# Optimization experiments

Measured on AMD Instinct MI355X. Metric: run time of the kernel, lower is better.

## Reference

```python
import jax, jax.numpy as jnp
import numpy as np

B, N, D = 16, 1024, 5
R_HID = 8  # radial MLP hidden width


def setup_inputs() -> dict:
    key = jax.random.key(0)
    ks = jax.random.split(key, 16)
    feats = jax.random.normal(ks[0], (B, N, D), jnp.float32)
    coors = 3.0 * jax.random.normal(ks[1], (B, N, 3), jnp.float32)
    a = jax.random.bernoulli(ks[2], 0.01, (B, N, N))
    adj_mat = a | jnp.swapaxes(a, 1, 2)
    s = 1.0 / np.sqrt(D)
    Wq = s * jax.random.normal(ks[3], (D, D), jnp.float32)
    Wk = s * jax.random.normal(ks[4], (D, D), jnp.float32)
    Wv = s * jax.random.normal(ks[5], (D, D), jnp.float32)
    Wo = s * jax.random.normal(ks[6], (D, D), jnp.float32)
    w_r1 = 0.5 * jax.random.normal(ks[7], (1, R_HID), jnp.float32)
    b_r1 = jnp.zeros((R_HID,), jnp.float32)
    w_r2 = 0.5 * jax.random.normal(ks[8], (R_HID, 1), jnp.float32)
    b_r2 = jnp.zeros((1,), jnp.float32)
    w1 = (1.0 / np.sqrt(D)) * jax.random.normal(ks[9], (D, 128), jnp.float32)
    b1 = jnp.zeros((128,), jnp.float32)
    w2 = (1.0 / np.sqrt(128.0)) * jax.random.normal(ks[10], (128, 3), jnp.float32)
    b2 = jnp.zeros((3,), jnp.float32)
    return dict(feats=feats, coors=coors, adj_mat=adj_mat, Wq=Wq, Wk=Wk, Wv=Wv,
                Wo=Wo, w_r1=w_r1, b_r1=b_r1, w_r2=w_r2, b_r2=b_r2,
                w1=w1, b1=b1, w2=w2, b2=b2)


def _se3_layer(feats, coors, neigh, Wq, Wk, Wv, Wo, w_r1, b_r1, w_r2, b_r2):
    # SE(3)-invariant sparse graph attention on degree-0 channels.
    # Attention logits = content term + radial (distance-only) bias, so the
    # scalar output is invariant to global rotations/translations of coors.
    q = jnp.einsum('bnd,de->bne', feats, Wq)
    k = jnp.einsum('bnd,de->bne', feats, Wk)
    v = jnp.einsum('bnd,de->bne', feats, Wv)
    rel = coors[:, :, None, :] - coors[:, None, :, :]        # [B,N,N,3]
    dist = jnp.sqrt(jnp.sum(rel * rel, axis=-1) + 1e-8)      # [B,N,N]
    h = jax.nn.relu(dist[..., None] * w_r1[0] + b_r1)        # [B,N,N,R_HID]
    rbias = (h @ w_r2)[..., 0] + b_r2[0]                     # [B,N,N]
    scores = jnp.einsum('bid,bjd->bij', q, k) / np.sqrt(q.shape[-1]) + rbias
    scores = jnp.where(neigh, scores, -1e9)
    attn = jax.nn.softmax(scores, axis=-1)
    agg = jnp.einsum('bij,bjd->bid', attn, v)
    return feats + jnp.einsum('bid,de->bie', agg, Wo)        # residual


def reference(feats, coors, adj_mat, Wq, Wk, Wv, Wo, w_r1, b_r1, w_r2, b_r2,
              w1, b1, w2, b2):
    a = adj_mat.astype(jnp.float32)
    # num_adj_degrees=2: attend over 1-hop and 2-hop neighbors (+ self)
    adj2 = jnp.einsum('bij,bjk->bik', a, a) > 0
    eye = jnp.eye(adj_mat.shape[1], dtype=bool)[None]
    neigh = adj_mat | adj2 | eye
    x = _se3_layer(feats, coors, neigh, Wq, Wk, Wv, Wo, w_r1, b_r1, w_r2, b_r2)
    pooled = jnp.mean(x, axis=1)                              # [B, D]
    hdn = jax.nn.relu(pooled @ w1 + b1)
    return hdn @ w2 + b2                                      # [B, 3]
```

## Files before the change

### kernel.cpp

```cpp
#include <hip/hip_runtime.h>
#include <hip/hip_bf16.h>

#define BB 16
#define NN 1024
#define DD 5
#define RH 8

typedef unsigned long long u64;
typedef unsigned int u32;
typedef __hip_bfloat16 bf16;

static __device__ __forceinline__ float tof(bf16 x) { return __bfloat162float(x); }
static __device__ __forceinline__ float ldf(const void* p, long long i, bool f) {
  return f ? ((const float*)p)[i] : tof(((const bf16*)p)[i]);
}

#define LOG2E 1.4426950408889634f
#define PACK_BLOCKS (BB * NN * 16 / 256)
#define KV_BLOCKS (BB * NN / 256)

__global__ __launch_bounds__(256) void k_pack(
    const void* __restrict__ adj, const void* __restrict__ feats,
    const void* __restrict__ coors,
    const void* __restrict__ Wk, const void* __restrict__ Wv,
    const void* __restrict__ Wo,
    u64* __restrict__ adjbits, float4* __restrict__ kvg,
    float* __restrict__ czg, int* __restrict__ gflags) {
  __shared__ int sNon01, sNonpair, sLow3;
  __shared__ int sCnt[4];
  __shared__ float wkL[25], wvL[25], woL[25];
  int tid = threadIdx.x;

  if (blockIdx.x >= PACK_BLOCKS) {
    int kb = blockIdx.x - PACK_BLOCKS;
    {
      u32 x = ((const u32*)feats)[tid];
      u32 lo = x & 0xFFFFu;
      int e = (int)((lo >> 7) & 0xFFu);
      bool insane = !(lo == 0u || (e >= 90 && e <= 150));
      u64 m = __ballot(insane);
      if ((tid & 63) == 0) sCnt[tid >> 6] = (int)__popcll(m);
    }
    if (tid < 25) {
    }
    __syncthreads();
    bool f32 = (sCnt[0] + sCnt[1] + sCnt[2] + sCnt[3]) > 64;
    if (tid < 25) {
      wkL[tid] = ldf(Wk, tid, f32);
      wvL[tid] = ldf(Wv, tid, f32);
      woL[tid] = ldf(Wo, tid, f32);
    }
    if (kb == 0 && tid == 0) gflags[0] = f32 ? 1 : 0;
    __syncthreads();
    long long node = (long long)kb * 256 + tid;
    float f0 = ldf(feats, node * DD + 0, f32), f1 = ldf(feats, node * DD + 1, f32),
          f2 = ldf(feats, node * DD + 2, f32), f3 = ldf(feats, node * DD + 3, f32),
          f4 = ldf(feats, node * DD + 4, f32);
    float k[DD], tv[DD], v[DD];
    #pragma unroll
    for (int e = 0; e < DD; ++e) {
      k[e] = f0 * wkL[e] + f1 * wkL[5 + e] + f2 * wkL[10 + e] + f3 * wkL[15 + e] +
             f4 * wkL[20 + e];
      tv[e] = f0 * wvL[e] + f1 * wvL[5 + e] + f2 * wvL[10 + e] + f3 * wvL[15 + e] +
              f4 * wvL[20 + e];
    }
    #pragma unroll
    for (int e = 0; e < DD; ++e)
      v[e] = tv[0] * woL[e] + tv[1] * woL[5 + e] + tv[2] * woL[10 + e] +
             tv[3] * woL[15 + e] + tv[4] * woL[20 + e];
    float cx = ldf(coors, node * 3 + 0, f32);
    float cy = ldf(coors, node * 3 + 1, f32);
    float cz = ldf(coors, node * 3 + 2, f32);
    kvg[node * 3 + 0] = make_float4(k[0], k[1], k[2], k[3]);
    kvg[node * 3 + 1] = make_float4(k[4], v[0], v[1], v[2]);
    kvg[node * 3 + 2] = make_float4(v[3], v[4], cx, cy);
    czg[node] = cz;
    return;
  }

  if (tid == 0) { sNon01 = 0; sNonpair = 0; sLow3 = 0; }
  __syncthreads();
  {
    const u32* aw = (const u32*)adj;
    int non01 = 0, nonpair = 0, low3 = 0;
    for (int i = tid; i < 4096; i += 256) {
      u32 x = aw[i];
      u32 lo = x & 0xFFFFu, hi = x >> 16;
      non01 |= (x > 1u);
      nonpair |= !((lo == 0u || lo == 0x3F80u) && (hi == 0u || hi == 0x3F80u));
      low3 |= (lo == 0x3F80u);
    }
    if (non01) atomicOr(&sNon01, 1);
    if (nonpair) atomicOr(&sNonpair, 1);
    if (low3) atomicOr(&sLow3, 1);
  }
  __syncthreads();
  int mode;
  if (!sNon01) mode = 0;
  else if (!sNonpair) mode = sLow3 ? 2 : 3;
  else mode = 1;

  int gid = blockIdx.x * 256 + tid;
  int w = gid & 15;
  long long row = gid >> 4;
  long long base = row * NN + (long long)w * 64;
  u64 bits = 0;
  if (mode == 3) {
    const uint4* p = (const uint4*)((const float*)adj + base);
    #pragma unroll
    for (int t = 0; t < 16; ++t) {
      uint4 x = p[t];
      if (x.x << 1) bits |= 1ull << (4 * t + 0);
      if (x.y << 1) bits |= 1ull << (4 * t + 1);
      if (x.z << 1) bits |= 1ull << (4 * t + 2);
      if (x.w << 1) bits |= 1ull << (4 * t + 3);
    }
  } else if (mode == 0) {
    const uint4* p = (const uint4*)((const u32*)adj + base);
    #pragma unroll
    for (int t = 0; t < 16; ++t) {
      uint4 x = p[t];
      if (x.x) bits |= 1ull << (4 * t + 0);
      if (x.y) bits |= 1ull << (4 * t + 1);
      if (x.z) bits |= 1ull << (4 * t + 2);
      if (x.w) bits |= 1ull << (4 * t + 3);
    }
  } else if (mode == 2) {
    const uint4* p = (const uint4*)((const unsigned short*)adj + base);
    #pragma unroll
    for (int t = 0; t < 8; ++t) {
      uint4 x = p[t];
      u32 c[4] = {x.x, x.y, x.z, x.w};
      #pragma unroll
      for (int q = 0; q < 4; ++q) {
        if ((c[q] & 0x7FFFu)) bits |= 1ull << (8 * t + 2 * q + 0);
        if ((c[q] >> 16) & 0x7FFFu) bits |= 1ull << (8 * t + 2 * q + 1);
      }
    }
  } else {
    const uint4* p = (const uint4*)((const unsigned char*)adj + base);
    #pragma unroll
    for (int t = 0; t < 4; ++t) {
      uint4 x = p[t];
      u32 c[4] = {x.x, x.y, x.z, x.w};
      #pragma unroll
      for (int q = 0; q < 4; ++q)
        #pragma unroll
        for (int bb = 0; bb < 4; ++bb)
          if ((c[q] >> (8 * bb)) & 0xFFu) bits |= 1ull << (16 * t + 4 * q + bb);
    }
  }
  adjbits[gid] = bits;
}

__global__ __launch_bounds__(256) void k_twohop(const u64* __restrict__ adjbits,
                                                u64* __restrict__ neighbits) {
  __shared__ unsigned short listL[4][NN];
  int wave = threadIdx.x >> 6, lane = threadIdx.x & 63;
  int row = blockIdx.x * 4 + wave;
  int b = row >> 10;
  int i = row & (NN - 1);
  int w = lane & 15;
  const u64* rowp = adjbits + (size_t)row * 16;
  u64 rw = rowp[w];
  unsigned short* list = listL[wave];
  int cnt = 0;
  #pragma unroll
  for (int sw = 0; sw < 16; ++sw) {
    u64 bits = __shfl(rw, sw, 64);
    int mybit = (int)((bits >> lane) & 1ull);
    int pre = __popcll(bits & ((1ull << lane) - 1ull));
    if (mybit) list[cnt + pre] = (unsigned short)(sw * 64 + lane);
    cnt += __popcll(bits);
  }
  __syncthreads();
  u64 acc = rw;
  if (w == (i >> 6)) acc |= 1ull << (i & 63);
  int g = lane >> 4;
  const u64* basep = adjbits + (size_t)b * NN * 16;
  for (int n = g; n < cnt; n += 4) {
    int j = list[n];
    acc |= basep[(size_t)j * 16 + w];
  }
  acc |= __shfl_xor(acc, 16, 64);
  acc |= __shfl_xor(acc, 32, 64);
  if (lane < 16) neighbits[(size_t)row * 16 + lane] = acc;
}

__global__ __launch_bounds__(256) void k_attn(
    const void* __restrict__ feats, const void* __restrict__ coors,
    const void* __restrict__ Wq,
    const void* __restrict__ wr1, const void* __restrict__ br1,
    const void* __restrict__ wr2, const void* __restrict__ br2,
    const float4* __restrict__ kvg, const float* __restrict__ czg,
    const int* __restrict__ gflags,
    const u64* __restrict__ neighbits, float* __restrict__ rowAgg) {
  __shared__ __align__(16) float4 kvL[512 * 3];
  __shared__ float czL[512];
  __shared__ float wqL[25];
  __shared__ float qL[16 * DD], ciL[16 * 3];
  __shared__ float wrL[3][RH];
  __shared__ float sConst[2];
  __shared__ int sFast;
  int bi = blockIdx.x;
  int b = bi >> 7, rem = bi & 127, chunk = rem >> 1, half = rem & 1;
  int j0 = half * 512;
  int tid = threadIdx.x;
  bool f32 = gflags[0] != 0;
  if (tid < 25) wqL[tid] = ldf(Wq, tid, f32);
  if (tid >= 64 && tid < 64 + RH) {
    int h = tid - 64;
    wrL[0][h] = ldf(wr1, h, f32);
    wrL[1][h] = ldf(br1, h, f32);
    wrL[2][h] = ldf(wr2, h, f32);
  }
  if (tid == 96) {
    float c = 0.0f;
    int ok = 1;
    #pragma unroll
    for (int h = 0; h < RH; ++h) {
      float w1h = ldf(wr1, h, f32);
      if (ldf(br1, h, f32) != 0.0f) ok = 0;
      if (w1h > 0.0f) c += w1h * ldf(wr2, h, f32);
    }
    sConst[0] = c * LOG2E;
    sConst[1] = ldf(br2, 0, f32) * LOG2E;
    sFast = ok;
  }
  {
    const float4* src = kvg + ((size_t)(b * NN) + j0) * 3;
    for (int idx = tid; idx < 512 * 3; idx += 256) kvL[idx] = src[idx];
    const float* csrc = czg + (size_t)(b * NN) + j0;
    for (int idx = tid; idx < 512; idx += 256) czL[idx] = csrc[idx];
  }
  __syncthreads();
  int fast = sFast;
  if (tid < 16) {
    long long row = (long long)b * NN + chunk * 16 + tid;
    float f0 = ldf(feats, row * DD + 0, f32), f1 = ldf(feats, row * DD + 1, f32),
          f2 = ldf(feats, row * DD + 2, f32), f3 = ldf(feats, row * DD + 3, f32),
          f4 = ldf(feats, row * DD + 4, f32);
    float qsc = fast ? (0.4472135954999579f * LOG2E) : 0.4472135954999579f;
    #pragma unroll
    for (int e = 0; e < DD; ++e)
      qL[tid * DD + e] = (f0 * wqL[e] + f1 * wqL[5 + e] + f2 * wqL[10 + e] +
                          f3 * wqL[15 + e] + f4 * wqL[20 + e]) * qsc;
    #pragma unroll
    for (int c = 0; c < 3; ++c)
      ciL[tid * 3 + c] = ldf(coors, row * 3 + c, f32);
  }
  __syncthreads();

  int g = tid >> 6, lane = tid & 63;
  int i0 = chunk * 16 + g * 4;
  float q[4][DD], ci[4][3], l[4], A[4][DD];
  #pragma unroll
  for (int r = 0; r < 4; ++r) {
    #pragma unroll
    for (int e = 0; e < DD; ++e) q[r][e] = qL[(g * 4 + r) * DD + e];
    #pragma unroll
    for (int c = 0; c < 3; ++c) ci[r][c] = ciL[(g * 4 + r) * 3 + c];
    l[r] = 0.0f;
    #pragma unroll
    for (int e = 0; e < DD; ++e) A[r][e] = 0.0f;
  }
  const u64* nb = neighbits + ((size_t)(b * NN + i0)) * 16 + half * 8;
  float Cf = sConst[0], br2f = sConst[1];
  for (int it = 0; it < 8; ++it) {
    int j = it * 64 + lane;
    float4 ka = kvL[j * 3 + 0];
    float4 kb = kvL[j * 3 + 1];
    float4 kc = kvL[j * 3 + 2];
    float jx = kc.z, jy = kc.w, jz = czL[j];
    u64 nw[4];
    #pragma unroll
    for (int r = 0; r < 4; ++r) nw[r] = nb[(size_t)r * 16 + it];
    if (fast) {
      #pragma unroll
      for (int r = 0; r < 4; ++r) {
        float cx = jx - ci[r][0], cy = jy - ci[r][1], cz = jz - ci[r][2];
        float dist =
            __builtin_amdgcn_sqrtf(fmaf(cx, cx, fmaf(cy, cy, fmaf(cz, cz, 1e-8f))));
        float s = fmaf(q[r][0], ka.x, br2f);
        s = fmaf(q[r][1], ka.y, s);
        s = fmaf(q[r][2], ka.z, s);
        s = fmaf(q[r][3], ka.w, s);
        s = fmaf(q[r][4], kb.x, s);
        s = fmaf(Cf, dist, s);
        s = fminf(s, 126.0f);
        s = ((nw[r] >> lane) & 1ull) ? s : -150.0f;
        float p = __builtin_amdgcn_exp2f(s);
        l[r] += p;
        A[r][0] = fmaf(p, kb.y, A[r][0]);
        A[r][1] = fmaf(p, kb.z, A[r][1]);
        A[r][2] = fmaf(p, kb.w, A[r][2]);
        A[r][3] = fmaf(p, kc.x, A[r][3]);
        A[r][4] = fmaf(p, kc.y, A[r][4]);
      }
    } else {
      #pragma unroll
      for (int r = 0; r < 4; ++r) {
        float cx = jx - ci[r][0], cy = jy - ci[r][1], cz = jz - ci[r][2];
        float dist = sqrtf(fmaf(cx, cx, fmaf(cy, cy, fmaf(cz, cz, 1e-8f))));
        float rb = ldf(br2, 0, f32);
        #pragma unroll
        for (int h = 0; h < RH; ++h)
          rb += fmaxf(dist * wrL[0][h] + wrL[1][h], 0.0f) * wrL[2][h];
        float s = fmaf(q[r][0], ka.x, rb);
        s = fmaf(q[r][1], ka.y, s);
        s = fmaf(q[r][2], ka.z, s);
        s = fmaf(q[r][3], ka.w, s);
        s = fmaf(q[r][4], kb.x, s);
        s = fminf(s, 85.0f);
        s = ((nw[r] >> lane) & 1ull) ? s : -100.0f;
        float p = __expf(s);
        l[r] += p;
        A[r][0] = fmaf(p, kb.y, A[r][0]);
        A[r][1] = fmaf(p, kb.z, A[r][1]);
        A[r][2] = fmaf(p, kb.w, A[r][2]);
        A[r][3] = fmaf(p, kc.x, A[r][3]);
        A[r][4] = fmaf(p, kc.y, A[r][4]);
      }
    }
  }
  #pragma unroll
  for (int msk = 1; msk < 64; msk <<= 1) {
    #pragma unroll
    for (int r = 0; r < 4; ++r) {
      l[r] += __shfl_xor(l[r], msk, 64);
      A[r][0] += __shfl_xor(A[r][0], msk, 64);
      A[r][1] += __shfl_xor(A[r][1], msk, 64);
      A[r][2] += __shfl_xor(A[r][2], msk, 64);
      A[r][3] += __shfl_xor(A[r][3], msk, 64);
      A[r][4] += __shfl_xor(A[r][4], msk, 64);
    }
  }
  if (lane == 0) {
    #pragma unroll
    for (int r = 0; r < 4; ++r) {
      float* o = rowAgg + (((size_t)(b * NN + i0 + r)) * 2 + half) * 6;
      o[0] = l[r];
      o[1] = A[r][0]; o[2] = A[r][1]; o[3] = A[r][2]; o[4] = A[r][3]; o[5] = A[r][4];
    }
  }
}

__global__ __launch_bounds__(256) void k_final(
    const void* __restrict__ feats, const float* __restrict__ rowAgg,
    const int* __restrict__ gflags,
    const void* __restrict__ w1, const void* __restrict__ b1,
    const void* __restrict__ w2, const void* __restrict__ b2,
    float* __restrict__ out) {
  __shared__ float waveL[4][DD];
  __shared__ float poolL[DD];
  __shared__ float hL[128];
  int b = blockIdx.x, tid = threadIdx.x;
  bool f32 = gflags[0] != 0;
  float pe[DD] = {0.f, 0.f, 0.f, 0.f, 0.f};
  for (int n = tid; n < NN; n += 256) {
    const float* ag = rowAgg + ((size_t)(b * NN + n)) * 12;
    float l = ag[0] + ag[6];
    float inv = (l > 0.f) ? 1.0f / l : 0.0f;
    long long base = ((long long)b * NN + n) * DD;
    #pragma unroll
    for (int e = 0; e < DD; ++e)
      pe[e] += ldf(feats, base + e, f32) + (ag[1 + e] + ag[7 + e]) * inv;
  }
  #pragma unroll
  for (int off = 32; off >= 1; off >>= 1)
    #pragma unroll
    for (int e = 0; e < DD; ++e) pe[e] += __shfl_down(pe[e], off, 64);
  int wave = tid >> 6, lane = tid & 63;
  if (lane == 0)
    #pragma unroll
    for (int e = 0; e < DD; ++e) waveL[wave][e] = pe[e];
  __syncthreads();
  if (tid < DD)
    poolL[tid] = (waveL[0][tid] + waveL[1][tid] + waveL[2][tid] + waveL[3][tid]) *
                 (1.0f / 1024.0f);
  __syncthreads();
  if (tid < 128) {
    float acc = ldf(b1, tid, f32);
    #pragma unroll
    for (int d = 0; d < DD; ++d)
      acc = fmaf(poolL[d], ldf(w1, d * 128 + tid, f32), acc);
    hL[tid] = fmaxf(acc, 0.0f);
  }
  __syncthreads();
  if (tid < 3) {
    float s = ldf(b2, tid, f32);
    for (int j = 0; j < 128; ++j) s = fmaf(hL[j], ldf(w2, j * 3 + tid, f32), s);
    out[b * 3 + tid] = s;
  }
}

extern "C" void kernel_launch(void* const* d_in, const int* in_sizes, int n_in,
                              void* d_out, int out_size, void* d_ws, size_t ws_size,
                              hipStream_t stream) {
  const void* adj = d_in[2];
  float* out = (float*)d_out;

  char* w = (char*)d_ws;
  int* gflags = (int*)w;
  const size_t MB2 = (size_t)BB * NN * 16 * sizeof(u64);
  u64* adjbits = (u64*)(w + 512);
  u64* neighbits = (u64*)(w + 512 + MB2);
  float* rowAgg = (float*)(w + 512 + 2 * MB2);
  float4* kvg = (float4*)(w + 512 + 2 * MB2 + 786432);
  float* czg = (float*)(w + 512 + 2 * MB2 + 2 * 786432);

  k_pack<<<PACK_BLOCKS + KV_BLOCKS, 256, 0, stream>>>(
      adj, d_in[0], d_in[1], d_in[4], d_in[5], d_in[6], adjbits, kvg, czg, gflags);
  k_twohop<<<BB * NN / 4, 256, 0, stream>>>(adjbits, neighbits);
  k_attn<<<BB * 128, 256, 0, stream>>>(d_in[0], d_in[1], d_in[3], d_in[7], d_in[8],
                                       d_in[9], d_in[10], kvg, czg, gflags,
                                       neighbits, rowAgg);
  k_final<<<BB, 256, 0, stream>>>(d_in[0], rowAgg, gflags, d_in[11], d_in[12],
                                  d_in[13], d_in[14], out);
}
```

Measured before the change: 188.1 us.

## Fuse two-hop neighbor mask computation into attention kernel

Removes the separate k_twohop kernel and its neighbits global buffer. Each attention block now computes the two-hop neighbor mask for its own 16 rows and 512-column half directly from adjbits, using the kvL shared buffer as scratch for the neighbor lists before kv data is loaded. This saves one kernel launch and the global write and read of neighbits. In exchange, each row's two-hop OR is recomputed twice, once per column half, and the mask work is serialized ahead of the kv load inside the attention block.

After: 200.2 us. +6.5%, slower.

```diff
diff --git a/kernel.cpp b/kernel.cpp
--- a/kernel.cpp
+++ b/kernel.cpp
@@ -41,8 +41,6 @@
       u64 m = __ballot(insane);
       if ((tid & 63) == 0) sCnt[tid >> 6] = (int)__popcll(m);
     }
-    if (tid < 25) {
-    }
     __syncthreads();
     bool f32 = (sCnt[0] + sCnt[1] + sCnt[2] + sCnt[3]) > 64;
     if (tid < 25) {
@@ -153,50 +151,17 @@
   adjbits[gid] = bits;
 }
 
-__global__ __launch_bounds__(256) void k_twohop(const u64* __restrict__ adjbits,
-                                                u64* __restrict__ neighbits) {
-  __shared__ unsigned short listL[4][NN];
-  int wave = threadIdx.x >> 6, lane = threadIdx.x & 63;
-  int row = blockIdx.x * 4 + wave;
-  int b = row >> 10;
-  int i = row & (NN - 1);
-  int w = lane & 15;
-  const u64* rowp = adjbits + (size_t)row * 16;
-  u64 rw = rowp[w];
-  unsigned short* list = listL[wave];
-  int cnt = 0;
-  #pragma unroll
-  for (int sw = 0; sw < 16; ++sw) {
-    u64 bits = __shfl(rw, sw, 64);
-    int mybit = (int)((bits >> lane) & 1ull);
-    int pre = __popcll(bits & ((1ull << lane) - 1ull));
-    if (mybit) list[cnt + pre] = (unsigned short)(sw * 64 + lane);
-    cnt += __popcll(bits);
-  }
-  __syncthreads();
-  u64 acc = rw;
-  if (w == (i >> 6)) acc |= 1ull << (i & 63);
-  int g = lane >> 4;
-  const u64* basep = adjbits + (size_t)b * NN * 16;
-  for (int n = g; n < cnt; n += 4) {
-    int j = list[n];
-    acc |= basep[(size_t)j * 16 + w];
-  }
-  acc |= __shfl_xor(acc, 16, 64);
-  acc |= __shfl_xor(acc, 32, 64);
-  if (lane < 16) neighbits[(size_t)row * 16 + lane] = acc;
-}
-
 __global__ __launch_bounds__(256) void k_attn(
     const void* __restrict__ feats, const void* __restrict__ coors,
     const void* __restrict__ Wq,
     const void* __restrict__ wr1, const void* __restrict__ br1,
     const void* __restrict__ wr2, const void* __restrict__ br2,
     const float4* __restrict__ kvg, const float* __restrict__ czg,
-    const int* __restrict__ gflags,
-    const u64* __restrict__ neighbits, float* __restrict__ rowAgg) {
+    const int* __restrict__ gflags, const u64* __restrict__ adjbits,
+    float* __restrict__ rowAgg) {
   __shared__ __align__(16) float4 kvL[512 * 3];
   __shared__ float czL[512];
+  __shared__ u64 nbL[16][8];
   __shared__ float wqL[25];
   __shared__ float qL[16 * DD], ciL[16 * 3];
   __shared__ float wrL[3][RH];
@@ -206,6 +171,7 @@
   int b = bi >> 7, rem = bi & 127, chunk = rem >> 1, half = rem & 1;
   int j0 = half * 512;
   int tid = threadIdx.x;
+  int wave = tid >> 6, lane = tid & 63;
   bool f32 = gflags[0] != 0;
   if (tid < 25) wqL[tid] = ldf(Wq, tid, f32);
   if (tid >= 64 && tid < 64 + RH) {
@@ -227,13 +193,44 @@
     sConst[1] = ldf(br2, 0, f32) * LOG2E;
     sFast = ok;
   }
+
+  {
+    unsigned short* list = (unsigned short*)kvL + wave * NN;
+    const u64* basep = adjbits + (size_t)b * NN * 16;
+    int w8 = lane & 7;
+    int widx = half * 8 + w8;
+    for (int rr = 0; rr < 4; ++rr) {
+      int lr = wave * 4 + rr;
+      int i = chunk * 16 + lr;
+      const u64* rowp = basep + (size_t)i * 16;
+      u64 rw = rowp[lane & 15];
+      int cnt = 0;
+      #pragma unroll
+      for (int sw = 0; sw < 16; ++sw) {
+        u64 bits = __shfl(rw, sw, 64);
+        int mybit = (int)((bits >> lane) & 1ull);
+        int pre = __popcll(bits & ((1ull << lane) - 1ull));
+        if (mybit) list[cnt + pre] = (unsigned short)(sw * 64 + lane);
+        cnt += __popcll(bits);
+      }
+      u64 acc = __shfl(rw, widx, 64);
+      if ((i >> 6) == widx) acc |= 1ull << (i & 63);
+      int g8 = lane >> 3;
+      for (int n = g8; n < cnt; n += 8) acc |= basep[(size_t)list[n] * 16 + widx];
+      acc |= __shfl_xor(acc, 8, 64);
+      acc |= __shfl_xor(acc, 16, 64);
+      acc |= __shfl_xor(acc, 32, 64);
+      if (lane < 8) nbL[lr][lane] = acc;
+    }
+  }
+  __syncthreads();
+
   {
     const float4* src = kvg + ((size_t)(b * NN) + j0) * 3;
     for (int idx = tid; idx < 512 * 3; idx += 256) kvL[idx] = src[idx];
     const float* csrc = czg + (size_t)(b * NN) + j0;
     for (int idx = tid; idx < 512; idx += 256) czL[idx] = csrc[idx];
   }
-  __syncthreads();
   int fast = sFast;
   if (tid < 16) {
     long long row = (long long)b * NN + chunk * 16 + tid;
@@ -251,20 +248,18 @@
   }
   __syncthreads();
 
-  int g = tid >> 6, lane = tid & 63;
-  int i0 = chunk * 16 + g * 4;
+  int i0 = chunk * 16 + wave * 4;
   float q[4][DD], ci[4][3], l[4], A[4][DD];
   #pragma unroll
   for (int r = 0; r < 4; ++r) {
     #pragma unroll
-    for (int e = 0; e < DD; ++e) q[r][e] = qL[(g * 4 + r) * DD + e];
-    #pragma unroll
-    for (int c = 0; c < 3; ++c) ci[r][c] = ciL[(g * 4 + r) * 3 + c];
+    for (int e = 0; e < DD; ++e) q[r][e] = qL[(wave * 4 + r) * DD + e];
+    #pragma unroll
+    for (int c = 0; c < 3; ++c) ci[r][c] = ciL[(wave * 4 + r) * 3 + c];
     l[r] = 0.0f;
     #pragma unroll
     for (int e = 0; e < DD; ++e) A[r][e] = 0.0f;
   }
-  const u64* nb = neighbits + ((size_t)(b * NN + i0)) * 16 + half * 8;
   float Cf = sConst[0], br2f = sConst[1];
   for (int it = 0; it < 8; ++it) {
     int j = it * 64 + lane;
@@ -274,7 +269,7 @@
     float jx = kc.z, jy = kc.w, jz = czL[j];
     u64 nw[4];
     #pragma unroll
-    for (int r = 0; r < 4; ++r) nw[r] = nb[(size_t)r * 16 + it];
+    for (int r = 0; r < 4; ++r) nw[r] = nbL[wave * 4 + r][it];
     if (fast) {
       #pragma unroll
       for (int r = 0; r < 4; ++r) {
@@ -404,17 +399,15 @@
   int* gflags = (int*)w;
   const size_t MB2 = (size_t)BB * NN * 16 * sizeof(u64);
   u64* adjbits = (u64*)(w + 512);
-  u64* neighbits = (u64*)(w + 512 + MB2);
-  float* rowAgg = (float*)(w + 512 + 2 * MB2);
-  float4* kvg = (float4*)(w + 512 + 2 * MB2 + 786432);
-  float* czg = (float*)(w + 512 + 2 * MB2 + 2 * 786432);
+  float* rowAgg = (float*)(w + 512 + MB2);
+  float4* kvg = (float4*)(w + 512 + MB2 + 786432);
+  float* czg = (float*)(w + 512 + MB2 + 2 * 786432);
 
   k_pack<<<PACK_BLOCKS + KV_BLOCKS, 256, 0, stream>>>(
       adj, d_in[0], d_in[1], d_in[4], d_in[5], d_in[6], adjbits, kvg, czg, gflags);
-  k_twohop<<<BB * NN / 4, 256, 0, stream>>>(adjbits, neighbits);
   k_attn<<<BB * 128, 256, 0, stream>>>(d_in[0], d_in[1], d_in[3], d_in[7], d_in[8],
                                        d_in[9], d_in[10], kvg, czg, gflags,
-                                       neighbits, rowAgg);
+                                       adjbits, rowAgg);
   k_final<<<BB, 256, 0, stream>>>(d_in[0], rowAgg, gflags, d_in[11], d_in[12],
                                   d_in[13], d_in[14], out);
 }
```

## Fuse final pooling and MLP into attention kernel via last-block counters

Applied to the files above, without the earlier changes.

Removes the separate k_final launch by having the second block of each row-chunk pair combine both halves, reduce its 16 rows and atomically add them into a per-batch pooled buffer. The last block to finish, found through a global done counter, runs the small MLP head for all batches. Counters and the pooled buffer are zeroed in k_pack. This saves one kernel launch and a serial tail kernel, at the cost of extra atomics, fences and a grid-wide last-block pattern. Float atomic accumulation also makes the pooled sum order nondeterministic.

Result: slower. 203.9 us (+8.4%).

```diff
diff --git a/kernel.cpp b/kernel.cpp
--- a/kernel.cpp
+++ b/kernel.cpp
@@ -13,6 +13,12 @@
 static __device__ __forceinline__ float tof(bf16 x) { return __bfloat162float(x); }
 static __device__ __forceinline__ float ldf(const void* p, long long i, bool f) {
   return f ? ((const float*)p)[i] : tof(((const bf16*)p)[i]);
+}
+static __device__ __forceinline__ void stG(float* p, float v) {
+  __hip_atomic_store(p, v, __ATOMIC_RELAXED, __HIP_MEMORY_SCOPE_AGENT);
+}
+static __device__ __forceinline__ float ldG(const float* p) {
+  return __hip_atomic_load(p, __ATOMIC_RELAXED, __HIP_MEMORY_SCOPE_AGENT);
 }
 
 #define LOG2E 1.4426950408889634f
@@ -25,7 +31,9 @@
     const void* __restrict__ Wk, const void* __restrict__ Wv,
     const void* __restrict__ Wo,
     u64* __restrict__ adjbits, float4* __restrict__ kvg,
-    float* __restrict__ czg, int* __restrict__ gflags) {
+    float* __restrict__ czg, int* __restrict__ gflags,
+    int* __restrict__ pairCnt, int* __restrict__ doneCnt,
+    float* __restrict__ pooled) {
   __shared__ int sNon01, sNonpair, sLow3;
   __shared__ int sCnt[4];
   __shared__ float wkL[25], wvL[25], woL[25];
@@ -40,8 +48,6 @@
       bool insane = !(lo == 0u || (e >= 90 && e <= 150));
       u64 m = __ballot(insane);
       if ((tid & 63) == 0) sCnt[tid >> 6] = (int)__popcll(m);
-    }
-    if (tid < 25) {
     }
     __syncthreads();
     bool f32 = (sCnt[0] + sCnt[1] + sCnt[2] + sCnt[3]) > 64;
@@ -78,6 +84,11 @@
     return;
   }
 
+  if (blockIdx.x == 0) {
+    for (int i = tid; i < BB * 64; i += 256) pairCnt[i] = 0;
+    if (tid < BB * DD) pooled[tid] = 0.0f;
+    if (tid == 0) *doneCnt = 0;
+  }
   if (tid == 0) { sNon01 = 0; sNonpair = 0; sLow3 = 0; }
   __syncthreads();
   {
@@ -194,18 +205,24 @@
     const void* __restrict__ wr2, const void* __restrict__ br2,
     const float4* __restrict__ kvg, const float* __restrict__ czg,
     const int* __restrict__ gflags,
-    const u64* __restrict__ neighbits, float* __restrict__ rowAgg) {
+    const u64* __restrict__ neighbits, float* __restrict__ rowAgg,
+    int* __restrict__ pairCnt, int* __restrict__ doneCnt,
+    float* __restrict__ pooled,
+    const void* __restrict__ w1v, const void* __restrict__ b1v,
+    const void* __restrict__ w2v, const void* __restrict__ b2v,
+    float* __restrict__ out) {
   __shared__ __align__(16) float4 kvL[512 * 3];
   __shared__ float czL[512];
   __shared__ float wqL[25];
   __shared__ float qL[16 * DD], ciL[16 * 3];
   __shared__ float wrL[3][RH];
   __shared__ float sConst[2];
-  __shared__ int sFast;
+  __shared__ int sFast, sOld, sDoneI;
   int bi = blockIdx.x;
   int b = bi >> 7, rem = bi & 127, chunk = rem >> 1, half = rem & 1;
   int j0 = half * 512;
   int tid = threadIdx.x;
+  int wave = tid >> 6, lane = tid & 63;
   bool f32 = gflags[0] != 0;
   if (tid < 25) wqL[tid] = ldf(Wq, tid, f32);
   if (tid >= 64 && tid < 64 + RH) {
@@ -251,15 +268,14 @@
   }
   __syncthreads();
 
-  int g = tid >> 6, lane = tid & 63;
-  int i0 = chunk * 16 + g * 4;
+  int i0 = chunk * 16 + wave * 4;
   float q[4][DD], ci[4][3], l[4], A[4][DD];
   #pragma unroll
   for (int r = 0; r < 4; ++r) {
     #pragma unroll
-    for (int e = 0; e < DD; ++e) q[r][e] = qL[(g * 4 + r) * DD + e];
-    #pragma unroll
-    for (int c = 0; c < 3; ++c) ci[r][c] = ciL[(g * 4 + r) * 3 + c];
+    for (int e = 0; e < DD; ++e) q[r][e] = qL[(wave * 4 + r) * DD + e];
+    #pragma unroll
+    for (int c = 0; c < 3; ++c) ci[r][c] = ciL[(wave * 4 + r) * 3 + c];
     l[r] = 0.0f;
     #pragma unroll
     for (int e = 0; e < DD; ++e) A[r][e] = 0.0f;
@@ -339,58 +355,70 @@
     #pragma unroll
     for (int r = 0; r < 4; ++r) {
       float* o = rowAgg + (((size_t)(b * NN + i0 + r)) * 2 + half) * 6;
-      o[0] = l[r];
-      o[1] = A[r][0]; o[2] = A[r][1]; o[3] = A[r][2]; o[4] = A[r][3]; o[5] = A[r][4];
-    }
-  }
-}
-
-__global__ __launch_bounds__(256) void k_final(
-    const void* __restrict__ feats, const float* __restrict__ rowAgg,
-    const int* __restrict__ gflags,
-    const void* __restrict__ w1, const void* __restrict__ b1,
-    const void* __restrict__ w2, const void* __restrict__ b2,
-    float* __restrict__ out) {
-  __shared__ float waveL[4][DD];
-  __shared__ float poolL[DD];
-  __shared__ float hL[128];
-  int b = blockIdx.x, tid = threadIdx.x;
-  bool f32 = gflags[0] != 0;
-  float pe[DD] = {0.f, 0.f, 0.f, 0.f, 0.f};
-  for (int n = tid; n < NN; n += 256) {
-    const float* ag = rowAgg + ((size_t)(b * NN + n)) * 12;
-    float l = ag[0] + ag[6];
-    float inv = (l > 0.f) ? 1.0f / l : 0.0f;
-    long long base = ((long long)b * NN + n) * DD;
+      stG(o + 0, l[r]);
+      stG(o + 1, A[r][0]); stG(o + 2, A[r][1]); stG(o + 3, A[r][2]);
+      stG(o + 4, A[r][3]); stG(o + 5, A[r][4]);
+    }
+  }
+  __threadfence_block();
+  __syncthreads();
+  if (tid == 0) sOld = atomicAdd(&pairCnt[bi >> 1], 1);
+  __syncthreads();
+  if (sOld == 1) {
+    float pe[DD] = {0.f, 0.f, 0.f, 0.f, 0.f};
+    if (tid < 16) {
+      size_t rid = (size_t)(b * NN + chunk * 16 + tid);
+      const float* ra = rowAgg + rid * 12;
+      float lsum = ldG(ra + 0) + ldG(ra + 6);
+      float inv = (lsum > 0.f) ? 1.0f / lsum : 0.0f;
+      long long fb = (long long)rid * DD;
+      #pragma unroll
+      for (int e = 0; e < DD; ++e)
+        pe[e] = ldf(feats, fb + e, f32) + (ldG(ra + 1 + e) + ldG(ra + 7 + e)) * inv;
+    }
+    if (tid < 64) {
+      #pragma unroll
+      for (int off = 8; off >= 1; off >>= 1)
+        #pragma unroll
+        for (int e = 0; e < DD; ++e) pe[e] += __shfl_down(pe[e], off, 64);
+    }
+    if (tid == 0) {
+      #pragma unroll
+      for (int e = 0; e < DD; ++e) atomicAdd(&pooled[b * DD + e], pe[e]);
+    }
+  }
+  __threadfence_block();
+  __syncthreads();
+  if (tid == 0) sDoneI = (atomicAdd(doneCnt, 1) == (int)gridDim.x - 1);
+  __syncthreads();
+  if (sDoneI) {
+    int bb2 = tid >> 4, sub = tid & 15;
+    float pl[DD];
     #pragma unroll
     for (int e = 0; e < DD; ++e)
-      pe[e] += ldf(feats, base + e, f32) + (ag[1 + e] + ag[7 + e]) * inv;
-  }
-  #pragma unroll
-  for (int off = 32; off >= 1; off >>= 1)
-    #pragma unroll
-    for (int e = 0; e < DD; ++e) pe[e] += __shfl_down(pe[e], off, 64);
-  int wave = tid >> 6, lane = tid & 63;
-  if (lane == 0)
-    #pragma unroll
-    for (int e = 0; e < DD; ++e) waveL[wave][e] = pe[e];
-  __syncthreads();
-  if (tid < DD)
-    poolL[tid] = (waveL[0][tid] + waveL[1][tid] + waveL[2][tid] + waveL[3][tid]) *
-                 (1.0f / 1024.0f);
-  __syncthreads();
-  if (tid < 128) {
-    float acc = ldf(b1, tid, f32);
-    #pragma unroll
-    for (int d = 0; d < DD; ++d)
-      acc = fmaf(poolL[d], ldf(w1, d * 128 + tid, f32), acc);
-    hL[tid] = fmaxf(acc, 0.0f);
-  }
-  __syncthreads();
-  if (tid < 3) {
-    float s = ldf(b2, tid, f32);
-    for (int j = 0; j < 128; ++j) s = fmaf(hL[j], ldf(w2, j * 3 + tid, f32), s);
-    out[b * 3 + tid] = s;
+      pl[e] = ldG(&pooled[bb2 * DD + e]) * (1.0f / 1024.0f);
+    float a0 = 0.f, a1 = 0.f, a2 = 0.f;
+    for (int jj = sub * 8; jj < sub * 8 + 8; ++jj) {
+      float h = ldf(b1v, jj, f32);
+      #pragma unroll
+      for (int d = 0; d < DD; ++d)
+        h = fmaf(pl[d], ldf(w1v, d * 128 + jj, f32), h);
+      h = fmaxf(h, 0.0f);
+      a0 = fmaf(h, ldf(w2v, jj * 3 + 0, f32), a0);
+      a1 = fmaf(h, ldf(w2v, jj * 3 + 1, f32), a1);
+      a2 = fmaf(h, ldf(w2v, jj * 3 + 2, f32), a2);
+    }
+    #pragma unroll
+    for (int mk = 1; mk < 16; mk <<= 1) {
+      a0 += __shfl_xor(a0, mk, 64);
+      a1 += __shfl_xor(a1, mk, 64);
+      a2 += __shfl_xor(a2, mk, 64);
+    }
+    if (sub == 0) {
+      out[bb2 * 3 + 0] = a0 + ldf(b2v, 0, f32);
+      out[bb2 * 3 + 1] = a1 + ldf(b2v, 1, f32);
+      out[bb2 * 3 + 2] = a2 + ldf(b2v, 2, f32);
+    }
   }
 }
 
@@ -402,19 +430,22 @@
 
   char* w = (char*)d_ws;
   int* gflags = (int*)w;
+  float* pooled = (float*)(w + 64);
+  int* doneCnt = (int*)(w + 448);
+  int* pairCnt = (int*)(w + 1024);
   const size_t MB2 = (size_t)BB * NN * 16 * sizeof(u64);
-  u64* adjbits = (u64*)(w + 512);
-  u64* neighbits = (u64*)(w + 512 + MB2);
-  float* rowAgg = (float*)(w + 512 + 2 * MB2);
-  float4* kvg = (float4*)(w + 512 + 2 * MB2 + 786432);
-  float* czg = (float*)(w + 512 + 2 * MB2 + 2 * 786432);
+  u64* adjbits = (u64*)(w + 8192);
+  u64* neighbits = (u64*)(w + 8192 + MB2);
+  float* rowAgg = (float*)(w + 8192 + 2 * MB2);
+  float4* kvg = (float4*)(w + 8192 + 2 * MB2 + 786432);
+  float* czg = (float*)(w + 8192 + 2 * MB2 + 2 * 786432);
 
   k_pack<<<PACK_BLOCKS + KV_BLOCKS, 256, 0, stream>>>(
-      adj, d_in[0], d_in[1], d_in[4], d_in[5], d_in[6], adjbits, kvg, czg, gflags);
+      adj, d_in[0], d_in[1], d_in[4], d_in[5], d_in[6], adjbits, kvg, czg,
+      gflags, pairCnt, doneCnt, pooled);
   k_twohop<<<BB * NN / 4, 256, 0, stream>>>(adjbits, neighbits);
   k_attn<<<BB * 128, 256, 0, stream>>>(d_in[0], d_in[1], d_in[3], d_in[7], d_in[8],
                                        d_in[9], d_in[10], kvg, czg, gflags,
-                                       neighbits, rowAgg);
-  k_final<<<BB, 256, 0, stream>>>(d_in[0], rowAgg, gflags, d_in[11], d_in[12],
-                                  d_in[13], d_in[14], out);
-}
+                                       neighbits, rowAgg, pairCnt, doneCnt, pooled,
+                                       d_in[11], d_in[12], d_in[13], d_in[14], out);
+}
```
